# Optimization experiments

Hardware: AMD Instinct MI355X
Metric: run time of the kernel (lower is better)

## Reference

```python
import jax, jax.numpy as jnp
import numpy as np

NUM_HEADS = 16
WINDOW = 128


def apply_rope(x):
    # x: (B, H, S, Dh), standard RoPE with half-split rotation, base 10000
    S, Dh = x.shape[-2], x.shape[-1]
    half = Dh // 2
    inv_freq = 1.0 / (10000.0 ** (jnp.arange(half, dtype=jnp.float32) / half))
    ang = jnp.arange(S, dtype=jnp.float32)[:, None] * inv_freq[None, :]  # (S, half)
    cos, sin = jnp.cos(ang), jnp.sin(ang)
    x1, x2 = x[..., :half], x[..., half:]
    return jnp.concatenate([x1 * cos - x2 * sin, x1 * sin + x2 * cos], axis=-1).astype(x.dtype)


def setup_inputs() -> dict:
    key = jax.random.key(0)
    ks = jax.random.split(key, 5)
    D = 1024
    B, S = 2, 2048
    w = 0.02
    return {
        "x": jax.random.normal(ks[0], (B, S, D), dtype=jnp.float32),
        "Wq": jax.random.normal(ks[1], (D, D), dtype=jnp.float32) * w,
        "bq": jnp.zeros((D,), dtype=jnp.float32),
        "Wk": jax.random.normal(ks[2], (D, D), dtype=jnp.float32) * w,
        "bk": jnp.zeros((D,), dtype=jnp.float32),
        "Wv": jax.random.normal(ks[3], (D, D), dtype=jnp.float32) * w,
        "bv": jnp.zeros((D,), dtype=jnp.float32),
        "Wo": jax.random.normal(ks[4], (D, D), dtype=jnp.float32) * w,
        "bo": jnp.zeros((D,), dtype=jnp.float32),
    }


def reference(x, Wq, bq, Wk, bk, Wv, bv, Wo, bo):
    B, S, D = x.shape
    H = NUM_HEADS
    Dh = D // H

    def proj(W, b):
        y = jnp.einsum("bsd,ed->bse", x, W) + b  # nn.Linear: x @ W.T + b
        return y.reshape(B, S, H, Dh).transpose(0, 2, 1, 3)  # (B,H,S,Dh)

    q = apply_rope(proj(Wq, bq)) * (Dh ** -0.5)
    k = apply_rope(proj(Wk, bk))
    v = proj(Wv, bv)

    scores = jnp.einsum("bhqd,bhkd->bhqk", q, k)  # (B,H,S,S)
    idx = jnp.arange(S)
    rel = idx[None, :] - idx[:, None]  # k - q
    blocked = (rel > 0) | (rel < -WINDOW)  # True = masked out
    scores = jnp.where(blocked[None, None], -jnp.inf, scores)
    probs = jax.nn.softmax(scores, axis=-1)
    out = jnp.einsum("bhqk,bhkd->bhqd", probs, v)
    out = out.transpose(0, 2, 1, 3).reshape(B, S, D)
    return jnp.einsum("bsd,ed->bse", out, Wo) + bo
```

## Files before the change

kernel.cpp:

```cpp
#include <hip/hip_runtime.h>

typedef __attribute__((ext_vector_type(8)))  __bf16 bf16x8;
typedef __attribute__((ext_vector_type(4)))  float  f32x4;

__device__ __forceinline__ short f2bf(float f) {
    unsigned u = __builtin_bit_cast(unsigned, f);
    unsigned r = (u + 0x7fffu + ((u >> 16) & 1u)) >> 16;
    return (short)r;
}
__device__ __forceinline__ float lo16(unsigned u) { return __builtin_bit_cast(float, u << 16); }
__device__ __forceinline__ float hi16(unsigned u) { return __builtin_bit_cast(float, u & 0xffff0000u); }

__device__ __forceinline__ void gload16(const void* g, void* l) {
    __builtin_amdgcn_global_load_lds(
        (const __attribute__((address_space(1))) unsigned*)g,
        (__attribute__((address_space(3))) unsigned*)l, 16, 0, 0);
}

__device__ __forceinline__ void ropePair(const uint4& a, const uint4& b,
                                         const float2* cs8, float scale,
                                         uint4& oa, uint4& ob) {
    const unsigned au[4] = {a.x, a.y, a.z, a.w}, bu[4] = {b.x, b.y, b.z, b.w};
    unsigned ra[4], rb[4];
    #pragma unroll
    for (int wi = 0; wi < 4; ++wi) {
        const float x1l = lo16(au[wi]), x1h = hi16(au[wi]);
        const float x2l = lo16(bu[wi]), x2h = hi16(bu[wi]);
        const float2 cl = cs8[wi * 2], ch = cs8[wi * 2 + 1];
        const float o1l = (x1l * cl.x - x2l * cl.y) * scale;
        const float o2l = (x1l * cl.y + x2l * cl.x) * scale;
        const float o1h = (x1h * ch.x - x2h * ch.y) * scale;
        const float o2h = (x1h * ch.y + x2h * ch.x) * scale;
        ra[wi] = (unsigned)(unsigned short)f2bf(o1l) | ((unsigned)(unsigned short)f2bf(o1h) << 16);
        rb[wi] = (unsigned)(unsigned short)f2bf(o2l) | ((unsigned)(unsigned short)f2bf(o2h) << 16);
    }
    oa = make_uint4(ra[0], ra[1], ra[2], ra[3]);
    ob = make_uint4(rb[0], rb[1], rb[2], rb[3]);
}

#define S_LEN   2048
#define MAT_ELEMS 4194304
#define VT_ROW  2176
#define VT_MAT  2228224

__global__ __launch_bounds__(256) void prep(
    const float* __restrict__ x,  const float* __restrict__ Wq,
    const float* __restrict__ Wk, const float* __restrict__ Wv,
    const float* __restrict__ Wo, const float* __restrict__ bq,
    const float* __restrict__ bk, const float* __restrict__ bv,
    short* __restrict__ xb, short* __restrict__ wcat, short* __restrict__ wob,
    float* __restrict__ bcat, float2* __restrict__ tab, short* __restrict__ vt)
{
    const int tid = blockIdx.x * 256 + threadIdx.x;
    const float4* src;
    short* dst;
    if (tid < 1048576) {
        src = (const float4*)x + tid;  dst = xb + (size_t)tid * 4;
    } else if (tid < 1835008) {
        const int o = tid - 1048576;
        const int mat = o >> 18;
        const int wi  = o & 262143;
        const float* W = (mat == 0) ? Wq : (mat == 1) ? Wk : Wv;
        src = (const float4*)W + wi;  dst = wcat + (size_t)o * 4;
    } else {
        const int o = tid - 1835008;
        src = (const float4*)Wo + o;  dst = wob + (size_t)o * 4;
    }
    const float4 v = *src;
    short4 s4 = make_short4(f2bf(v.x), f2bf(v.y), f2bf(v.z), f2bf(v.w));
    *(short4*)dst = s4;

    if (tid < 65536) {
        const int s  = tid >> 5;
        const int jr = tid & 31;
        const float freq = exp2f(-(float)jr * (13.287712379549449f / 32.0f));
        const float ang  = (float)s * freq;
        tab[tid] = make_float2(cosf(ang), sinf(ang));
    }
    if (tid < 768) {
        const float* B = (tid < 256) ? bq : (tid < 512) ? bk : bv;
        ((float4*)bcat)[tid] = ((const float4*)B)[tid & 255];
    }
    if (tid < 16384) {
        const int row = tid >> 3, ch = tid & 7;
        *(uint4*)&vt[(size_t)row * VT_ROW + ch * 8] = make_uint4(0, 0, 0, 0);
    }
}

#define VMC4 do { asm volatile("s_waitcnt vmcnt(4)" ::: "memory"); __builtin_amdgcn_sched_barrier(0); } while (0)
#define VMC0 do { asm volatile("s_waitcnt vmcnt(0)" ::: "memory"); __builtin_amdgcn_sched_barrier(0); } while (0)
#define BAR  __builtin_amdgcn_s_barrier()

#define LOADA(T, PM)                                                      \
  _Pragma("unroll") for (int ii = 0; ii < 4; ++ii) {                      \
    af[ii][0] = ldf(T, fA0, (ii * 32 + (PM) * 128) * 128);                \
    af[ii][1] = ldf(T, fA1, (ii * 32 + (PM) * 128) * 128);                \
  }

#define LOADB(T, PN, BQ)                                                  \
  _Pragma("unroll") for (int jj = 0; jj < 2; ++jj) {                      \
    BQ[jj][0] = ldf(T, fB0, (jj * 64 + (PN) * 128) * 128);                \
    BQ[jj][1] = ldf(T, fB1, (jj * 64 + (PN) * 128) * 128);                \
  }

#define MFMAQ(PM, PN, BQ)                                                     \
  __builtin_amdgcn_s_setprio(1);                                              \
  _Pragma("unroll") for (int ii = 0; ii < 4; ++ii)                            \
    _Pragma("unroll") for (int jj = 0; jj < 2; ++jj) {                        \
      acc[(PM)*4+ii][(PN)*2+jj] = __builtin_amdgcn_mfma_f32_16x16x32_bf16(    \
          af[ii][0], BQ[jj][0], acc[(PM)*4+ii][(PN)*2+jj], 0, 0, 0);          \
      acc[(PM)*4+ii][(PN)*2+jj] = __builtin_amdgcn_mfma_f32_16x16x32_bf16(    \
          af[ii][1], BQ[jj][1], acc[(PM)*4+ii][(PN)*2+jj], 0, 0, 0);          \
    }                                                                         \
  __builtin_amdgcn_s_setprio(0);

#define KTILE(AC, BC, S1, S2, S3, S4, W4)                                 \
  LOADA(AC, 0); LOADB(BC, 0, bq0); S1; BAR; MFMAQ(0, 0, bq0); BAR;        \
  LOADB(BC, 1, bq1); S2; BAR; MFMAQ(0, 1, bq1); BAR;                      \
  LOADA(AC, 1); S3; BAR; MFMAQ(1, 0, bq0); BAR;                           \
  S4; BAR; MFMAQ(1, 1, bq1); W4; BAR;

#define STG(G, KT_, H, TILE)                                               \
  { gload16(G + (H) * 262144 + 0     + (KT_) * 128, TILE + ((H)*128 + w*16    ) * 64); \
    gload16(G + (H) * 262144 + 16384 + (KT_) * 128, TILE + ((H)*128 + w*16 + 8) * 64); }

__global__ __launch_bounds__(512) void gemm8(
    const short* __restrict__ A,
    const short* __restrict__ Bw,
    const float* __restrict__ bias,
    short* __restrict__ outb,
    short* __restrict__ vt)
{
    __shared__ short lds[65536];
    short* const Ab0 = lds;
    short* const Bb0 = lds + 16384;
    short* const Ab1 = lds + 32768;
    short* const Bb1 = lds + 49152;

    const int tid = threadIdx.x;
    const int w = tid >> 6, lane = tid & 63;
    const int wm = w >> 2, wn = w & 3;
    const int lr = lane & 15, lg = lane >> 4;

    const int wg  = blockIdx.x;
    const int swz = (wg & 7) * 24 + (wg >> 3);
    const int bx = swz % 12, by = swz / 12;
    const int row0 = by * 256, col0 = bx * 256;

    const int scl  = ((lane & 7) * 16) ^ (((lane >> 3) & 7) << 4);
    const int goff = (w * 16 + (lane >> 3)) * 2048 + scl;
    const char* gA = (const char*)A  + (size_t)row0 * 2048 + goff;
    const char* gB = (const char*)Bw + (size_t)col0 * 2048 + goff;
    const int cswz0 = (lg * 16)      ^ ((lr & 7) << 4);
    const int cswz1 = (64 + lg * 16) ^ ((lr & 7) << 4);
    const int fA0 = (wm * 16 + lr) * 128 + cswz0;
    const int fA1 = (wm * 16 + lr) * 128 + cswz1;
    const int fB0 = (wn * 16 + lr) * 128 + cswz0;
    const int fB1 = (wn * 16 + lr) * 128 + cswz1;

    auto ldf = [&](const short* buf, int voff, int imm) -> bf16x8 {
        return *(const bf16x8*)((const char*)buf + voff + imm);
    };

    f32x4 acc[8][4] = {};
    bf16x8 af[4][2], bq0[2][2], bq1[2][2];

    STG(gA, 0, 0, Ab0);  STG(gB, 0, 0, Bb0);
    STG(gA, 0, 1, Ab0);  STG(gB, 0, 1, Bb0);
    STG(gA, 1, 0, Ab1);  STG(gB, 1, 0, Bb1);
    VMC4;
    BAR;

    #pragma unroll 1
    for (int it = 0; it < 7; ++it) {
        const int t0 = it * 2;
        KTILE(Ab0, Bb0,
              STG(gA, t0 + 1, 1, Ab1),
              STG(gB, t0 + 1, 1, Bb1),
              STG(gA, t0 + 2, 0, Ab0),
              STG(gB, t0 + 2, 0, Bb0), VMC4);
        const int t1 = t0 + 1;
        KTILE(Ab1, Bb1,
              STG(gA, t1 + 1, 1, Ab0),
              STG(gB, t1 + 1, 1, Bb0),
              STG(gA, t1 + 2, 0, Ab1),
              STG(gB, t1 + 2, 0, Bb1), VMC4);
    }
    KTILE(Ab0, Bb0,
          STG(gA, 15, 1, Ab1),
          STG(gB, 15, 1, Bb1), {}, {}, VMC0);
    KTILE(Ab1, Bb1, {}, {}, {}, {}, {});

    const int mat = col0 >> 10;
    const int cm0 = col0 & 1023;
    if (mat == 2) {
        #pragma unroll
        for (int j = 0; j < 4; ++j) {
            const int co = wn * 16 + (j & 1) * 64 + (j >> 1) * 128 + lr;
            const float bb = bias[col0 + co];
            const size_t dgo = (size_t)(cm0 + co) * VT_ROW;
            #pragma unroll
            for (int i = 0; i < 8; ++i) {
                const int rg = row0 + wm * 16 + (i & 3) * 32 + (i >> 2) * 128 + lg * 4;
                const int bq_ = rg >> 11, key = rg & 2047;
                short4 sv;
                sv.x = f2bf(acc[i][j][0] + bb); sv.y = f2bf(acc[i][j][1] + bb);
                sv.z = f2bf(acc[i][j][2] + bb); sv.w = f2bf(acc[i][j][3] + bb);
                *(short4*)&vt[(size_t)bq_ * VT_MAT + dgo + 128 + key] = sv;
            }
        }
    } else {
        short* outm = outb + (size_t)mat * MAT_ELEMS;
        #pragma unroll
        for (int j = 0; j < 4; ++j) {
            const int co = wn * 16 + (j & 1) * 64 + (j >> 1) * 128 + lr;
            const float bb = bias[col0 + co];
            #pragma unroll
            for (int i = 0; i < 8; ++i) {
                const int rg = row0 + wm * 16 + (i & 3) * 32 + (i >> 2) * 128 + lg * 4;
                #pragma unroll
                for (int r = 0; r < 4; ++r)
                    outm[(size_t)(rg + r) * 1024 + cm0 + co] = f2bf(acc[i][j][r] + bb);
            }
        }
    }
}

__global__ __launch_bounds__(256) void gemm_out(
    const short* __restrict__ A, const short* __restrict__ Bw,
    const float* __restrict__ bias, float* __restrict__ outf)
{
    __shared__ short As[128 * 64];
    __shared__ short Bs[128 * 64];
    const int tid  = threadIdx.x;
    const int w    = tid >> 6, lane = tid & 63;
    const int row0 = blockIdx.y * 128, col0 = blockIdx.x * 128;
    const int wr   = w >> 1, wc = w & 1;
    const int lr   = lane & 15, lg = lane >> 4;
    const int srow = lane >> 3, scol = (lane & 7) * 8;

    f32x4 acc[4][4] = {};

    for (int kt = 0; kt < 16; ++kt) {
        const int k0 = kt * 64;
        __syncthreads();
        #pragma unroll
        for (int rr = 0; rr < 4; ++rr) {
            const int ch = w * 4 + rr;
            const int r  = ch * 8 + srow;
            gload16(A  + (size_t)(row0 + r) * 1024 + k0 + scol, (short*)As + ch * 512);
            gload16(Bw + (size_t)(col0 + r) * 1024 + k0 + scol, (short*)Bs + ch * 512);
        }
        __syncthreads();
        #pragma unroll
        for (int kk = 0; kk < 2; ++kk) {
            const int kb = kk * 32 + lg * 8;
            bf16x8 af[4], bf[4];
            #pragma unroll
            for (int i = 0; i < 4; ++i) {
                af[i] = *(const bf16x8*)&As[(wr * 64 + i * 16 + lr) * 64 + kb];
                bf[i] = *(const bf16x8*)&Bs[(wc * 64 + i * 16 + lr) * 64 + kb];
            }
            #pragma unroll
            for (int i = 0; i < 4; ++i)
                #pragma unroll
                for (int j = 0; j < 4; ++j)
                    acc[i][j] = __builtin_amdgcn_mfma_f32_16x16x32_bf16(af[i], bf[j], acc[i][j], 0, 0, 0);
        }
    }

    #pragma unroll
    for (int i = 0; i < 4; ++i) {
        const int grb = row0 + wr * 64 + i * 16 + lg * 4;
        #pragma unroll
        for (int j = 0; j < 4; ++j) {
            const int cm = col0 + wc * 64 + j * 16 + lr;
            const float bb = bias[cm];
            #pragma unroll
            for (int r = 0; r < 4; ++r)
                outf[(size_t)(grb + r) * 1024 + cm] = acc[i][j][r] + bb;
        }
    }
}

#define KS_ST 72
#define P_ST  168
__global__ __launch_bounds__(256) void attn_mfma(const short* __restrict__ qkv,
                                                 const short* __restrict__ vt,
                                                 short* __restrict__ ctx,
                                                 const float2* __restrict__ tab)
{
    __shared__ char lds[52736];
    short* Ks  = (short*)lds;
    short* Pl  = (short*)lds;
    char*  VTs = lds + 27648;
    float* linv = (float*)(lds + 52480);

    const int tid = threadIdx.x;
    const int w = tid >> 6, lane = tid & 63;
    const int g = lane >> 4, l15 = lane & 15;
    const int phys = blockIdx.x;
    const int bid = (phys & 7) * 128 + (phys >> 3);
    const int b  = bid >> 9;
    const int h  = (bid >> 5) & 15;
    const int qb = bid & 31;
    const int qs = qb << 6;
    const size_t rowbase = (size_t)b * S_LEN;
    const int hc = h << 6;

    const short* vhead = vt + ((size_t)b * 1024 + h * 64) * VT_ROW + qs;
    #pragma unroll
    for (int rdx = 0; rdx < 6; ++rdx) {
        const int c = rdx * 256 + tid;
        const int row = c / 24, ch = c - row * 24;
        const int srcb = (ch * 16) ^ ((row & 7) << 4);
        gload16((const char*)(vhead + (size_t)row * VT_ROW) + srcb, VTs + c * 16);
    }

    #pragma unroll
    for (int it = 0; it < 3; ++it) {
        const int c   = it * 256 + tid;
        const int key = c >> 2;
        const int jb  = (c & 3) << 3;
        const int gk  = qs - 128 + key;
        const int gkc = gk < 0 ? 0 : gk;
        const short* kb = qkv + (size_t)1 * MAT_ELEMS + (rowbase + gkc) * 1024 + hc;
        const uint4 k1 = *(const uint4*)(kb + jb);
        const uint4 k2 = *(const uint4*)(kb + jb + 32);
        uint4 o1, o2;
        ropePair(k1, k2, tab + (size_t)gkc * 32 + jb, 1.0f, o1, o2);
        if (gk < 0) { o1 = make_uint4(0, 0, 0, 0); o2 = make_uint4(0, 0, 0, 0); }
        *(uint4*)&Ks[key * KS_ST + jb]      = o1;
        *(uint4*)&Ks[key * KS_ST + jb + 32] = o2;
    }
    __syncthreads();

    const int q = qs + 16 * w + l15;
    const size_t qoff = (rowbase + q) * 1024 + hc;
    const uint4 q1 = *(const uint4*)&qkv[qoff + g * 8];
    const uint4 q2 = *(const uint4*)&qkv[qoff + 32 + g * 8];
    uint4 r1, r2;
    ropePair(q1, q2, tab + (size_t)q * 32 + g * 8, 0.125f, r1, r2);
    const bf16x8 qf0 = __builtin_bit_cast(bf16x8, r1);
    const bf16x8 qf1 = __builtin_bit_cast(bf16x8, r2);

    f32x4 st[9];
    #pragma unroll
    for (int t = 0; t < 9; ++t) {
        const int krow = 16 * w + 16 * t + l15;
        bf16x8 kf0 = *(const bf16x8*)&Ks[krow * KS_ST + g * 8];
        bf16x8 kf1 = *(const bf16x8*)&Ks[krow * KS_ST + 32 + g * 8];
        f32x4 a = {0.f, 0.f, 0.f, 0.f};
        a = __builtin_amdgcn_mfma_f32_16x16x32_bf16(qf0, kf0, a, 0, 0, 0);
        a = __builtin_amdgcn_mfma_f32_16x16x32_bf16(qf1, kf1, a, 0, 0, 0);
        st[t] = a;
    }
    __syncthreads();

    const int jmin = 128 - qs - 16 * w;
    float mrow[4], lsum[4];
    #pragma unroll
    for (int r = 0; r < 4; ++r) mrow[r] = -3.0e38f;
    #pragma unroll
    for (int t = 0; t < 9; ++t) {
        const int jj = 16 * t + l15;
        #pragma unroll
        for (int r = 0; r < 4; ++r) {
            const int qi = 4 * g + r;
            const bool ok = (jj >= qi) && (jj <= qi + 128) && (jj >= jmin);
            if (ok) mrow[r] = fmaxf(mrow[r], st[t][r]);
        }
    }
    #pragma unroll
    for (int r = 0; r < 4; ++r) {
        mrow[r] = fmaxf(mrow[r], __shfl_xor(mrow[r], 1));
        mrow[r] = fmaxf(mrow[r], __shfl_xor(mrow[r], 2));
        mrow[r] = fmaxf(mrow[r], __shfl_xor(mrow[r], 4));
        mrow[r] = fmaxf(mrow[r], __shfl_xor(mrow[r], 8));
        lsum[r] = 0.0f;
    }
    short* Pw = Pl + w * (16 * P_ST);
    #pragma unroll
    for (int t = 0; t < 9; ++t) {
        const int jj = 16 * t + l15;
        #pragma unroll
        for (int r = 0; r < 4; ++r) {
            const int qi = 4 * g + r;
            const bool ok = (jj >= qi) && (jj <= qi + 128) && (jj >= jmin);
            const float p = ok ? __expf(st[t][r] - mrow[r]) : 0.0f;
            lsum[r] += p;
            Pw[qi * P_ST + jj] = f2bf(p);
        }
    }
    {
        short4 z = make_short4(0, 0, 0, 0);
        *(short4*)&Pw[l15 * P_ST + 144 + 4 * g] = z;
    }
    #pragma unroll
    for (int r = 0; r < 4; ++r) {
        lsum[r] += __shfl_xor(lsum[r], 1);
        lsum[r] += __shfl_xor(lsum[r], 2);
        lsum[r] += __shfl_xor(lsum[r], 4);
        lsum[r] += __shfl_xor(lsum[r], 8);
        if (l15 == r) linv[w * 16 + 4 * g + r] = 1.0f / lsum[r];
    }

    f32x4 oc[4] = {};
    #pragma unroll
    for (int kc = 0; kc < 5; ++kc) {
        bf16x8 pf = *(const bf16x8*)&Pw[l15 * P_ST + kc * 32 + g * 8];
        const int colb = (16 * w + kc * 32 + g * 8) * 2;
        #pragma unroll
        for (int dt = 0; dt < 4; ++dt) {
            const int row = dt * 16 + l15;
            bf16x8 vf = *(const bf16x8*)(VTs + row * 384 + (colb ^ ((row & 7) << 4)));
            oc[dt] = __builtin_amdgcn_mfma_f32_16x16x32_bf16(vf, pf, oc[dt], 0, 0, 0);
        }
    }

    const float inv = linv[w * 16 + l15];
    #pragma unroll
    for (int dt = 0; dt < 4; ++dt) {
        short4 sv;
        sv.x = f2bf(oc[dt][0] * inv);
        sv.y = f2bf(oc[dt][1] * inv);
        sv.z = f2bf(oc[dt][2] * inv);
        sv.w = f2bf(oc[dt][3] * inv);
        *(short4*)&ctx[(rowbase + qs + 16 * w + l15) * 1024 + hc + dt * 16 + 4 * g] = sv;
    }
}

extern "C" void kernel_launch(void* const* d_in, const int* in_sizes, int n_in,
                              void* d_out, int out_size, void* d_ws, size_t ws_size,
                              hipStream_t stream) {
    const float* x  = (const float*)d_in[0];
    const float* Wq = (const float*)d_in[1];
    const float* bq = (const float*)d_in[2];
    const float* Wk = (const float*)d_in[3];
    const float* bk = (const float*)d_in[4];
    const float* Wv = (const float*)d_in[5];
    const float* bv = (const float*)d_in[6];
    const float* Wo = (const float*)d_in[7];
    const float* bo = (const float*)d_in[8];

    char* ws = (char*)d_ws;
    short*  xb   = (short*) (ws + 0);
    short*  ctx  = (short*) (ws + 0);
    short*  wcat = (short*) (ws + 8388608);
    short*  wob  = (short*) (ws + 14680064);
    short*  qkv  = (short*) (ws + 16777216);
    short*  vt   = (short*) (ws + 33554432);
    float2* tab  = (float2*)(ws + 42467328);
    float*  bcat = (float*) (ws + 42991616);

    prep<<<8192, 256, 0, stream>>>(x, Wq, Wk, Wv, Wo, bq, bk, bv,
                                   xb, wcat, wob, bcat, tab, vt);
    gemm8<<<192, 512, 0, stream>>>(xb, wcat, bcat, qkv, vt);
    attn_mfma<<<1024, 256, 0, stream>>>(qkv, vt, ctx, tab);
    gemm_out<<<dim3(8, 32), 256, 0, stream>>>(ctx, wob, bo, (float*)d_out);
}
```

Baseline: 92.89 us.

## Software-pipeline LDS fragment loads across MFMA quadrants and K-tiles in QKV GEMM

Restructures the GEMM inner loop so that LDS-to-register fragment loads for the next quadrant, and for the next K-tile's first quadrant, are issued right after the current MFMA block, with separate register sets for the A and B halves. This is meant to hide LDS read latency behind MFMA execution instead of stalling before each MFMA quadrant. It adds register pressure from double fragment buffers, which could hurt occupancy or cause spills, and it relies on sched_barriers and the existing barriers to keep the prefetched tile valid.

```diff
diff --git a/kernel.cpp b/kernel.cpp
--- a/kernel.cpp
+++ b/kernel.cpp
@@ -90,35 +90,37 @@
 #define VMC4 do { asm volatile("s_waitcnt vmcnt(4)" ::: "memory"); __builtin_amdgcn_sched_barrier(0); } while (0)
 #define VMC0 do { asm volatile("s_waitcnt vmcnt(0)" ::: "memory"); __builtin_amdgcn_sched_barrier(0); } while (0)
 #define BAR  __builtin_amdgcn_s_barrier()
-
-#define LOADA(T, PM)                                                      \
-  _Pragma("unroll") for (int ii = 0; ii < 4; ++ii) {                      \
-    af[ii][0] = ldf(T, fA0, (ii * 32 + (PM) * 128) * 128);                \
-    af[ii][1] = ldf(T, fA1, (ii * 32 + (PM) * 128) * 128);                \
-  }
-
-#define LOADB(T, PN, BQ)                                                  \
-  _Pragma("unroll") for (int jj = 0; jj < 2; ++jj) {                      \
-    BQ[jj][0] = ldf(T, fB0, (jj * 64 + (PN) * 128) * 128);                \
-    BQ[jj][1] = ldf(T, fB1, (jj * 64 + (PN) * 128) * 128);                \
-  }
-
-#define MFMAQ(PM, PN, BQ)                                                     \
+#define SB   __builtin_amdgcn_sched_barrier(0)
+
+#define LDA0(T) _Pragma("unroll") for (int ii = 0; ii < 4; ++ii) { \
+    aA[ii][0] = ldf(T, fA0, (ii * 32) * 128);                       \
+    aA[ii][1] = ldf(T, fA1, (ii * 32) * 128); }
+#define LDA1(T) _Pragma("unroll") for (int ii = 0; ii < 4; ++ii) { \
+    aB[ii][0] = ldf(T, fA0, (ii * 32 + 128) * 128);                 \
+    aB[ii][1] = ldf(T, fA1, (ii * 32 + 128) * 128); }
+#define LDB0(T) _Pragma("unroll") for (int jj = 0; jj < 2; ++jj) { \
+    bA[jj][0] = ldf(T, fB0, (jj * 64) * 128);                       \
+    bA[jj][1] = ldf(T, fB1, (jj * 64) * 128); }
+#define LDB1(T) _Pragma("unroll") for (int jj = 0; jj < 2; ++jj) { \
+    bB[jj][0] = ldf(T, fB0, (jj * 64 + 128) * 128);                 \
+    bB[jj][1] = ldf(T, fB1, (jj * 64 + 128) * 128); }
+
+#define MFQ(PM, PN, AF, BF)                                                   \
   __builtin_amdgcn_s_setprio(1);                                              \
   _Pragma("unroll") for (int ii = 0; ii < 4; ++ii)                            \
     _Pragma("unroll") for (int jj = 0; jj < 2; ++jj) {                        \
       acc[(PM)*4+ii][(PN)*2+jj] = __builtin_amdgcn_mfma_f32_16x16x32_bf16(    \
-          af[ii][0], BQ[jj][0], acc[(PM)*4+ii][(PN)*2+jj], 0, 0, 0);          \
+          AF[ii][0], BF[jj][0], acc[(PM)*4+ii][(PN)*2+jj], 0, 0, 0);          \
       acc[(PM)*4+ii][(PN)*2+jj] = __builtin_amdgcn_mfma_f32_16x16x32_bf16(    \
-          af[ii][1], BQ[jj][1], acc[(PM)*4+ii][(PN)*2+jj], 0, 0, 0);          \
+          AF[ii][1], BF[jj][1], acc[(PM)*4+ii][(PN)*2+jj], 0, 0, 0);          \
     }                                                                         \
   __builtin_amdgcn_s_setprio(0);
 
-#define KTILE(AC, BC, S1, S2, S3, S4, W4)                                 \
-  LOADA(AC, 0); LOADB(BC, 0, bq0); S1; BAR; MFMAQ(0, 0, bq0); BAR;        \
-  LOADB(BC, 1, bq1); S2; BAR; MFMAQ(0, 1, bq1); BAR;                      \
-  LOADA(AC, 1); S3; BAR; MFMAQ(1, 0, bq0); BAR;                           \
-  S4; BAR; MFMAQ(1, 1, bq1); W4; BAR;
+#define KTILE(AC, BC, AN, BN, S1, S2, S3, S4, W4)                         \
+  S1; BAR; MFQ(0, 0, aA, bA); SB; LDB1(BC); SB; BAR;                      \
+  S2; BAR; MFQ(0, 1, aA, bB); SB; LDA1(AC); SB; BAR;                      \
+  S3; BAR; MFQ(1, 0, aB, bA); SB; BAR;                                    \
+  S4; BAR; MFQ(1, 1, aB, bB); W4; SB; LDA0(AN); LDB0(BN); SB; BAR;
 
 #define STG(G, KT_, H, TILE)                                               \
   { gload16(G + (H) * 262144 + 0     + (KT_) * 128, TILE + ((H)*128 + w*16    ) * 64); \
@@ -163,33 +165,37 @@
     };
 
     f32x4 acc[8][4] = {};
-    bf16x8 af[4][2], bq0[2][2], bq1[2][2];
+    bf16x8 aA[4][2], aB[4][2], bA[2][2], bB[2][2];
 
     STG(gA, 0, 0, Ab0);  STG(gB, 0, 0, Bb0);
     STG(gA, 0, 1, Ab0);  STG(gB, 0, 1, Bb0);
     STG(gA, 1, 0, Ab1);  STG(gB, 1, 0, Bb1);
     VMC4;
     BAR;
+    LDA0(Ab0); LDB0(Bb0);
 
     #pragma unroll 1
     for (int it = 0; it < 7; ++it) {
         const int t0 = it * 2;
-        KTILE(Ab0, Bb0,
+        KTILE(Ab0, Bb0, Ab1, Bb1,
               STG(gA, t0 + 1, 1, Ab1),
               STG(gB, t0 + 1, 1, Bb1),
               STG(gA, t0 + 2, 0, Ab0),
               STG(gB, t0 + 2, 0, Bb0), VMC4);
         const int t1 = t0 + 1;
-        KTILE(Ab1, Bb1,
+        KTILE(Ab1, Bb1, Ab0, Bb0,
               STG(gA, t1 + 1, 1, Ab0),
               STG(gB, t1 + 1, 1, Bb0),
               STG(gA, t1 + 2, 0, Ab1),
               STG(gB, t1 + 2, 0, Bb1), VMC4);
     }
-    KTILE(Ab0, Bb0,
+    KTILE(Ab0, Bb0, Ab1, Bb1,
           STG(gA, 15, 1, Ab1),
           STG(gB, 15, 1, Bb1), {}, {}, VMC0);
-    KTILE(Ab1, Bb1, {}, {}, {}, {}, {});
+    MFQ(0, 0, aA, bA); SB; LDB1(Bb1); SB;
+    MFQ(0, 1, aA, bB); SB; LDA1(Ab1); SB;
+    MFQ(1, 0, aB, bA);
+    MFQ(1, 1, aB, bB);
 
     const int mat = col0 >> 10;
     const int cm0 = col0 & 1023;
```

New measurement: 93.16 us. No clear change (+0.3%).
